# Performance work log

Hardware: AMD Instinct MI355X
Metric: run time of the kernel (lower is better)

## Reference

```python
import jax, jax.numpy as jnp
import numpy as np

B, L, E = 2, 1024, 1024
H, D = 16, 64          # num_heads, head_dim; E == H*D
KS, PAD = 3, 1         # depthwise conv kernel / padding
PROB = 0.9             # bernoulli keep-prob for key mask
NEG = -1e20


def _group(x):
    # [b, l, (h d)] -> [b, h, l, d]
    b, l, _ = x.shape
    return x.reshape(b, l, H, D).transpose(0, 2, 1, 3)


def setup_inputs() -> dict:
    key = jax.random.key(0)
    ks = jax.random.split(key, 8)
    query = jax.random.normal(ks[0], (B, L, E), jnp.float32)
    keys = jax.random.normal(ks[1], (B, L, E), jnp.float32)
    values = jax.random.normal(ks[2], (B, L, E), jnp.float32)
    padding_mask = jnp.ones((B, L, L), dtype=bool)
    causal_mask = jnp.broadcast_to(jnp.tril(jnp.ones((L, L), dtype=bool)), (B, L, L))
    ber_mask = jax.random.bernoulli(ks[3], PROB, (B, L))
    conv_w = jax.random.normal(ks[4], (H, 1, KS, KS), jnp.float32) * 0.2
    conv_b = jnp.zeros((H,), jnp.float32)
    bn_gamma = jnp.ones((H,), jnp.float32)
    bn_beta = jnp.zeros((H,), jnp.float32)
    w_v = jax.random.normal(ks[5], (D, D), jnp.float32) / np.sqrt(D)
    ln_gamma = jnp.ones((D,), jnp.float32)
    ln_beta = jnp.zeros((D,), jnp.float32)
    w_o = jax.random.normal(ks[6], (D, D), jnp.float32) / np.sqrt(D)
    b_o = jnp.zeros((D,), jnp.float32)
    return dict(query=query, keys=keys, values=values, padding_mask=padding_mask,
                causal_mask=causal_mask, ber_mask=ber_mask, conv_w=conv_w,
                conv_b=conv_b, bn_gamma=bn_gamma, bn_beta=bn_beta, w_v=w_v,
                ln_gamma=ln_gamma, ln_beta=ln_beta, w_o=w_o, b_o=b_o)


def reference(query, keys, values, padding_mask, causal_mask, ber_mask,
              conv_w, conv_b, bn_gamma, bn_beta, w_v, ln_gamma, ln_beta, w_o, b_o):
    gelu = lambda x: jax.nn.gelu(x, approximate=False)  # torch nn.GELU default (erf)

    # ---- query path: depthwise conv + residual, BatchNorm2d (batch stats), GELU
    qg = _group(query)  # [b, h, l, d]
    qc = jax.lax.conv_general_dilated(
        qg, conv_w, window_strides=(1, 1), padding=[(PAD, PAD), (PAD, PAD)],
        feature_group_count=H, dimension_numbers=('NCHW', 'OIHW', 'NCHW'))
    qc = qc + conv_b[None, :, None, None] + qg
    mean = qc.mean(axis=(0, 2, 3), keepdims=True)
    var = qc.var(axis=(0, 2, 3), keepdims=True)  # biased, as torch BN training
    q = gelu((qc - mean) * jax.lax.rsqrt(var + 1e-5)
             * bn_gamma[None, :, None, None] + bn_beta[None, :, None, None])

    # ---- key path: bernoulli-masked softmax over sequence, then GELU
    km = jnp.where(ber_mask[:, :, None], keys, NEG)
    k = gelu(_group(jax.nn.softmax(km, axis=-2)))  # softmax over length

    # ---- value path: per-head linear (no bias)
    v = jnp.einsum('bhld,ed->bhle', _group(values), w_v)

    # ---- GELU attention with combined padding & causal mask
    energy = gelu(jnp.einsum('bhqd,bhkd->bhqk', q, k))
    mask = padding_mask & causal_mask  # [b, q, k]
    energy = jnp.where(mask[:, None, :, :], energy, NEG)
    attn = jax.nn.softmax(energy / np.sqrt(E), axis=-1)

    # ---- attend, LayerNorm over head_dim, (dropout=identity in eval), linear
    o = jnp.einsum('bhqk,bhkd->bhqd', attn, v)
    mu = o.mean(-1, keepdims=True)
    s2 = o.var(-1, keepdims=True)
    on = (o - mu) * jax.lax.rsqrt(s2 + 1e-5) * ln_gamma + ln_beta
    out = jnp.einsum('bhqd,ed->bhqe', on, w_o) + b_o
    # [b, h, l, d] -> [b, l, (h d)]
    return out.transpose(0, 2, 1, 3).reshape(B, L, E)
```

## Files before the change

### kernel.cpp

```cpp
#include <hip/hip_runtime.h>
#include <hip/hip_bf16.h>
#include <math.h>

#define BB 2
#define HH 16
#define LL 1024
#define DD 64
#define EE 1024
#define NEGV -1e20f

typedef __attribute__((ext_vector_type(8))) short bf16x8;
typedef __attribute__((ext_vector_type(4))) float f32x4;

__device__ __forceinline__ float bf2f(__hip_bfloat16 x){ return __bfloat162float(x); }
__device__ __forceinline__ float gelu_erf(float x){
    return 0.5f * x * (1.0f + erff(x * 0.70710678118654752f));
}
__device__ __forceinline__ float gelu_sig(float x){
    float e = __expf(-1.702f * x);
    return x * __builtin_amdgcn_rcpf(1.0f + e);
}
__device__ __forceinline__ float ldx(const void* p, size_t i, int f32){
    return f32 ? ((const float*)p)[i] : bf2f(((const __hip_bfloat16*)p)[i]);
}
__device__ __forceinline__ short f2bs(float x){
    __hip_bfloat16 h = __float2bfloat16(x);
    return *(short*)&h;
}
__device__ __forceinline__ float bs2f(unsigned short u){
    return __uint_as_float(((unsigned)u) << 16);
}
__device__ __forceinline__ bf16x8 ld8b(const void* p, size_t i, int f32){
    bf16x8 r;
    if (f32){
        const float4* f = (const float4*)((const float*)p + i);
        float4 a = f[0], b = f[1];
        r[0]=f2bs(a.x); r[1]=f2bs(a.y); r[2]=f2bs(a.z); r[3]=f2bs(a.w);
        r[4]=f2bs(b.x); r[5]=f2bs(b.y); r[6]=f2bs(b.z); r[7]=f2bs(b.w);
    } else {
        r = *(const bf16x8*)((const __hip_bfloat16*)p + i);
    }
    return r;
}
__device__ __forceinline__ float redsum16(float x){
    x += __shfl_xor(x, 1); x += __shfl_xor(x, 2);
    x += __shfl_xor(x, 4); x += __shfl_xor(x, 8);
    return x;
}
__device__ __forceinline__ int detect_f32_wave(const unsigned int* p, int lane){
    unsigned int e0 = (p[lane] >> 7) & 0xFFu;
    int inband = (e0 >= 0x60u && e0 <= 0x8Eu) ? 1 : 0;
    unsigned long long m = __ballot(inband);
    return (__popcll(m) >= 48) ? 0 : 1;
}
__device__ __forceinline__ int ber_code_wave(const unsigned char* r, int lane){
    int j0 = lane * 2, j1 = lane * 2 + 1;
    unsigned char c0 = r[j0], c1 = r[j1];
    int big = (c0 > 1) || (c1 > 1);
    int odd = (((j1 & 3) == 1) && c1) || (((j0 & 3) == 1) && c0);
    int nz  = (((j0 & 3) != 0) && c0) || (((j1 & 3) != 0) && c1);
    unsigned long long mb = __ballot(big);
    unsigned long long mo = __ballot(odd);
    unsigned long long mn = __ballot(nz);
    if (mb) return mo ? 2 : 3;
    return mn ? 0 : 1;
}
__device__ __forceinline__ float ber_val(const unsigned char* r, int i, int code){
    switch (code){
        case 0:  return r[i] ? 1.f : 0.f;
        case 1:  return (((const int*)r)[i] != 0) ? 1.f : 0.f;
        case 2:  return (((const unsigned short*)r)[i] != 0) ? 1.f : 0.f;
        default: return (((const float*)r)[i] != 0.f) ? 1.f : 0.f;
    }
}

__global__ __launch_bounds__(256, 2) void kA(const void* __restrict__ query,
                                             const void* __restrict__ conv_w,
                                             const void* __restrict__ conv_b,
                                             const void* __restrict__ keys,
                                             const void* __restrict__ values,
                                             const void* __restrict__ w_v,
                                             const unsigned char* __restrict__ ber_raw,
                                             float* __restrict__ statsP,
                                             float* __restrict__ Sp,
                                             float* __restrict__ berf,
                                             int* __restrict__ wsflag,
                                             __hip_bfloat16* __restrict__ qbf,
                                             __hip_bfloat16* __restrict__ vbT){
    __shared__ float tile[66][67];
    __shared__ float r1[256], r2[256];
    __shared__ float ss[4][64];
    int blk = blockIdx.x, t = threadIdx.x;
    int lane = t & 63;
    if (blk < 512){
        const int f32 = detect_f32_wave((const unsigned int*)query, lane);
        if (blk == 0 && t == 0) wsflag[0] = f32;
        int lt = blk & 15, h = (blk >> 4) & 15, b = blk >> 8;
        int bh = b * HH + h;
        int l0 = lt * 64;
        if (t < 66){ tile[t][0] = 0.f; tile[t][65] = 0.f; }
        __syncthreads();
        for (int i = t; i < 66 * 64; i += 256){
            int r = i >> 6, d = i & 63;
            int l = l0 - 1 + r;
            tile[r][d + 1] = (l >= 0 && l < LL)
                           ? ldx(query, ((size_t)b * LL + l) * EE + h * 64 + d, f32) : 0.f;
        }
        __syncthreads();
        float w9[9];
        #pragma unroll
        for (int i = 0; i < 9; ++i) w9[i] = ldx(conv_w, h * 9 + i, f32);
        float cb = ldx(conv_b, h, f32);
        int l = t & 63, db = t >> 6, d0 = db * 16;
        float s1 = 0.f, s2 = 0.f;
        unsigned short ob[16];
        #pragma unroll
        for (int jj = 0; jj < 16; ++jj){
            int d = d0 + jj;
            float acc = cb + tile[l + 1][d + 1];
            #pragma unroll
            for (int di = 0; di < 3; ++di)
                #pragma unroll
                for (int dj = 0; dj < 3; ++dj)
                    acc += w9[di * 3 + dj] * tile[l + di][d + dj];
            s1 += acc; s2 += acc * acc;
            ob[jj] = (unsigned short)f2bs(acc);
        }
        __hip_bfloat16* orow = qbf + ((size_t)bh * LL + l0 + l) * DD + d0;
        #pragma unroll
        for (int g = 0; g < 4; ++g){
            ushort4 u; u.x = ob[g*4]; u.y = ob[g*4+1]; u.z = ob[g*4+2]; u.w = ob[g*4+3];
            *(ushort4*)(orow + g * 4) = u;
        }
        r1[t] = s1; r2[t] = s2;
        __syncthreads();
        for (int s = 128; s > 0; s >>= 1){
            if (t < s){ r1[t] += r1[t + s]; r2[t] += r2[t + s]; }
            __syncthreads();
        }
        if (t == 0){
            statsP[h * 32 + b * 16 + lt] = r1[0];
            statsP[512 + h * 32 + b * 16 + lt] = r2[0];
        }
    } else if (blk < 1024){
        int blk2 = blk - 512;
        const int f32 = detect_f32_wave((const unsigned int*)keys, lane);
        const int code = ber_code_wave(ber_raw, lane);
        int ch = blk2 & 15, h = (blk2 >> 4) & 15, b = blk2 >> 8;
        int ex = t & 63, ly = t >> 6;
        int e = h * 64 + ex;
        float s = 0.f;
        #pragma unroll 4
        for (int l = ch * 64 + ly; l < ch * 64 + 64; l += 4){
            float keep = ber_val(ber_raw, b * LL + l, code);
            float x = (keep != 0.f) ? ldx(keys, ((size_t)b * LL + l) * EE + e, f32) : NEGV;
            s += __expf(x);
        }
        ss[ly][ex] = s;
        __syncthreads();
        if (ly == 0)
            Sp[(b * 16 + ch) * EE + e] = ss[0][ex] + ss[1][ex] + ss[2][ex] + ss[3][ex];
        if (h == 0 && t < 64)
            berf[b * LL + ch * 64 + t] = ber_val(ber_raw, b * LL + ch * 64 + t, code);
    } else {
        const int f32 = detect_f32_wave((const unsigned int*)values, lane);
        int blk2 = blk - 1024;
        int lt = blk2 & 15, bh = blk2 >> 4;
        int h = bh & 15, b = bh >> 4;
        int w = t >> 6;
        int lid = lane & 15, quad = lane >> 4;
        int l = lt * 64 + w * 16 + lid;
        bf16x8 av[2];
        #pragma unroll
        for (int ck = 0; ck < 2; ++ck)
            av[ck] = ld8b(values, ((size_t)b * LL + l) * EE + h * 64 + ck * 32 + quad * 8, f32);
        f32x4 Dv[4];
        #pragma unroll
        for (int et = 0; et < 4; ++et){
            Dv[et] = (f32x4){0.f, 0.f, 0.f, 0.f};
            #pragma unroll
            for (int ck = 0; ck < 2; ++ck){
                bf16x8 bw = ld8b(w_v, (size_t)(et * 16 + lid) * 64 + ck * 32 + quad * 8, f32);
                Dv[et] = __builtin_amdgcn_mfma_f32_16x16x32_bf16(av[ck], bw, Dv[et], 0, 0, 0);
            }
        }
        #pragma unroll
        for (int et = 0; et < 4; ++et){
            ushort4 u;
            u.x = (unsigned short)f2bs(Dv[et][0]);
            u.y = (unsigned short)f2bs(Dv[et][1]);
            u.z = (unsigned short)f2bs(Dv[et][2]);
            u.w = (unsigned short)f2bs(Dv[et][3]);
            *(ushort4*)(vbT + ((size_t)bh * DD + et * 16 + lid) * LL + lt * 64 + w * 16 + quad * 4) = u;
        }
    }
}

__global__ __launch_bounds__(256, 2) void kB(const void* __restrict__ keys,
                                             const void* __restrict__ bn_g,
                                             const void* __restrict__ bn_b,
                                             const float* __restrict__ statsP,
                                             const float* __restrict__ Sp,
                                             const float* __restrict__ berf,
                                             const int* __restrict__ wsflag,
                                             __hip_bfloat16* __restrict__ kb,
                                             float* __restrict__ coef){
    __shared__ float sinv_s[64];
    int blk = blockIdx.x, t = threadIdx.x;
    const int f32 = wsflag[0];
    if (blk == 0 && t < HH){
        int h = t;
        float s1 = 0.f, s2 = 0.f;
        #pragma unroll 1
        for (int j = 0; j < 32; ++j){
            s1 += statsP[h * 32 + j];
            s2 += statsP[512 + h * 32 + j];
        }
        const float N = (float)(BB * LL * DD);
        float mean = s1 / N;
        float var  = fmaxf(s2 / N - mean * mean, 0.f);
        float a = ldx(bn_g, h, f32) * rsqrtf(var + 1e-5f);
        coef[h] = a;
        coef[16 + h] = ldx(bn_b, h, f32) - mean * a;
    }
    int i8 = (blk * 256 + t) * 8;
    int d0 = i8 & 63, l = (i8 >> 6) & 1023, h = (i8 >> 16) & 15, b = i8 >> 20;
    if (t < 64){
        int e = h * 64 + t;
        float S = 0.f;
        #pragma unroll
        for (int ch = 0; ch < 16; ++ch) S += Sp[(b * 16 + ch) * EE + e];
        sinv_s[t] = 1.f / S;
    }
    __syncthreads();
    size_t kbase = ((size_t)b * LL + l) * EE + h * 64 + d0;
    float kv[8];
    if (f32){
        const float4* kp = (const float4*)((const float*)keys + kbase);
        float4 a = kp[0], c = kp[1];
        kv[0]=a.x; kv[1]=a.y; kv[2]=a.z; kv[3]=a.w;
        kv[4]=c.x; kv[5]=c.y; kv[6]=c.z; kv[7]=c.w;
    } else {
        uint4 kr = *(const uint4*)((const __hip_bfloat16*)keys + kbase);
        unsigned short* ks = (unsigned short*)&kr;
        #pragma unroll
        for (int j = 0; j < 8; ++j) kv[j] = bs2f(ks[j]);
    }
    float keep = berf[b * LL + l];
    uint4 kw;
    unsigned short* kws = (unsigned short*)&kw;
    #pragma unroll
    for (int j = 0; j < 8; ++j){
        float km = (keep != 0.f) ? kv[j] : NEGV;
        float p = __expf(km) * sinv_s[d0 + j];
        kws[j] = (unsigned short)f2bs(gelu_erf(p));
    }
    *(uint4*)(kb + i8) = kw;
}

__global__ __launch_bounds__(128, 4) void kD(const __hip_bfloat16* __restrict__ qbf,
                                             const __hip_bfloat16* __restrict__ kb,
                                             const __hip_bfloat16* __restrict__ vbT,
                                             const void* __restrict__ w_o,
                                             const void* __restrict__ b_o,
                                             const void* __restrict__ ln_g,
                                             const void* __restrict__ ln_b,
                                             const int* __restrict__ wsflag,
                                             const float* __restrict__ coef,
                                             void* __restrict__ out){
    __shared__ __align__(16) __hip_bfloat16 Pl[2][2][16][40];
    __shared__ __align__(16) float Ol[16][68];
    __shared__ __align__(16) __hip_bfloat16 onb[16][72];
    int blk = blockIdx.x;
    int qt = 63 - (blk >> 5);
    int bh = blk & 31;
    int h = bh & 15, b = bh >> 4;
    int t = threadIdx.x;
    int w = t >> 6, lane = t & 63;
    int lid = lane & 15, quad = lane >> 4;
    const int f32o = wsflag[0];

    int qrow = qt * 16 + lid;
    float bna = coef[h], bnc = coef[16 + h];
    bf16x8 qf[2];
    #pragma unroll
    for (int ck = 0; ck < 2; ++ck){
        bf16x8 raw = *(const bf16x8*)(qbf + ((size_t)bh * LL + qrow) * DD + ck * 32 + quad * 8);
        #pragma unroll
        for (int j = 0; j < 8; ++j)
            qf[ck][j] = f2bs(gelu_erf(bs2f((unsigned short)raw[j]) * bna + bnc));
    }

    const __hip_bfloat16* kbb = kb + (size_t)bh * LL * DD;
    const __hip_bfloat16* vbb = vbT + (size_t)bh * DD * LL;
    f32x4 O[4];
    #pragma unroll
    for (int nt = 0; nt < 4; ++nt) O[nt] = (f32x4){0.f, 0.f, 0.f, 0.f};
    const int qlane = qt * 16 + quad * 4;
    const int nkt = (qt >> 3) + 1;

    auto loadK = [&](int kw, bf16x8* dk){
        #pragma unroll
        for (int nt2 = 0; nt2 < 4; ++nt2)
            #pragma unroll
            for (int ck = 0; ck < 2; ++ck)
                dk[nt2 * 2 + ck] = *(const bf16x8*)(kbb
                    + (size_t)(kw + nt2 * 16 + lid) * DD + ck * 32 + quad * 8);
    };
    auto loadV = [&](int kw, bf16x8* dv){
        #pragma unroll
        for (int ks = 0; ks < 2; ++ks)
            #pragma unroll
            for (int nt = 0; nt < 4; ++nt)
                dv[ks * 4 + nt] = *(const bf16x8*)(vbb
                    + (size_t)(nt * 16 + lid) * LL + kw + ks * 32 + quad * 8);
    };

    bf16x8 kf[8], vf[8];
    loadK(w * 64, kf);
    loadV(w * 64, vf);

    for (int kt0 = 0; kt0 < nkt; ++kt0){
        int kw0 = kt0 * 128 + w * 64;
        const bool more = (kt0 + 1 < nkt);
        f32x4 S[4];
        #pragma unroll
        for (int nt2 = 0; nt2 < 4; ++nt2){
            S[nt2] = (f32x4){0.f, 0.f, 0.f, 0.f};
            #pragma unroll
            for (int ck = 0; ck < 2; ++ck)
                S[nt2] = __builtin_amdgcn_mfma_f32_16x16x32_bf16(qf[ck], kf[nt2 * 2 + ck], S[nt2], 0, 0, 0);
        }
        if (more) loadK((kt0 + 1) * 128 + w * 64, kf);
        #pragma unroll
        for (int nt2 = 0; nt2 < 4; ++nt2){
            int kcol = kw0 + nt2 * 16 + lid;
            #pragma unroll
            for (int r = 0; r < 4; ++r){
                float x = gelu_sig(S[nt2][r]) * 0.03125f;
                float p = __expf(x);
                p = (kcol <= qlane + r) ? p : 0.f;
                Pl[w][nt2 >> 1][quad * 4 + r][((nt2 & 1) << 4) + lid] = __float2bfloat16(p);
            }
        }
        bf16x8 pa0 = *(const bf16x8*)&Pl[w][0][lid][quad * 8];
        bf16x8 pa1 = *(const bf16x8*)&Pl[w][1][lid][quad * 8];
        #pragma unroll
        for (int nt = 0; nt < 4; ++nt)
            O[nt] = __builtin_amdgcn_mfma_f32_16x16x32_bf16(pa0, vf[nt], O[nt], 0, 0, 0);
        #pragma unroll
        for (int nt = 0; nt < 4; ++nt)
            O[nt] = __builtin_amdgcn_mfma_f32_16x16x32_bf16(pa1, vf[4 + nt], O[nt], 0, 0, 0);
        if (more) loadV((kt0 + 1) * 128 + w * 64, vf);
    }

    if (w == 1){
        #pragma unroll
        for (int nt = 0; nt < 4; ++nt)
            #pragma unroll
            for (int r = 0; r < 4; ++r)
                Ol[quad * 4 + r][nt * 16 + lid] = O[nt][r];
    }
    __syncthreads();
    if (w == 0){
        #pragma unroll
        for (int nt = 0; nt < 4; ++nt)
            #pragma unroll
            for (int r = 0; r < 4; ++r)
                O[nt][r] += Ol[quad * 4 + r][nt * 16 + lid];
        float lng_v[4], lnb_v[4];
        #pragma unroll
        for (int nt = 0; nt < 4; ++nt){
            lng_v[nt] = ldx(ln_g, nt * 16 + lid, f32o);
            lnb_v[nt] = ldx(ln_b, nt * 16 + lid, f32o);
        }
        #pragma unroll
        for (int r = 0; r < 4; ++r){
            float s = O[0][r] + O[1][r] + O[2][r] + O[3][r];
            s = redsum16(s);
            float mu = s * (1.f / 64.f);
            float vs = 0.f;
            #pragma unroll
            for (int nt = 0; nt < 4; ++nt){ float d2 = O[nt][r] - mu; vs += d2 * d2; }
            vs = redsum16(vs);
            float iv = rsqrtf(vs * (1.f / 64.f) + 1e-5f);
            #pragma unroll
            for (int nt = 0; nt < 4; ++nt){
                float on = (O[nt][r] - mu) * iv * lng_v[nt] + lnb_v[nt];
                onb[quad * 4 + r][nt * 16 + lid] = __float2bfloat16(on);
            }
        }
    }
    __syncthreads();
    bf16x8 oa0 = *(const bf16x8*)&onb[lid][quad * 8];
    bf16x8 oa1 = *(const bf16x8*)&onb[lid][32 + quad * 8];
    #pragma unroll
    for (int i = 0; i < 2; ++i){
        int et = w * 2 + i;
        float bo = ldx(b_o, et * 16 + lid, f32o);
        f32x4 R = (f32x4){bo, bo, bo, bo};
        bf16x8 bw0 = ld8b(w_o, (size_t)(et * 16 + lid) * 64 + quad * 8, f32o);
        bf16x8 bw1 = ld8b(w_o, (size_t)(et * 16 + lid) * 64 + 32 + quad * 8, f32o);
        R = __builtin_amdgcn_mfma_f32_16x16x32_bf16(oa0, bw0, R, 0, 0, 0);
        R = __builtin_amdgcn_mfma_f32_16x16x32_bf16(oa1, bw1, R, 0, 0, 0);
        #pragma unroll
        for (int r = 0; r < 4; ++r){
            size_t oidx = ((size_t)b * LL + qlane + r) * EE + h * 64 + et * 16 + lid;
            if (f32o) ((float*)out)[oidx] = R[r];
            else      ((__hip_bfloat16*)out)[oidx] = __float2bfloat16(R[r]);
        }
    }
}

extern "C" void kernel_launch(void* const* d_in, const int* in_sizes, int n_in,
                              void* d_out, int out_size, void* d_ws, size_t ws_size,
                              hipStream_t stream){
    int iq=-1, ik=-1, iv=-1, iber=-1, icw=-1, icb=-1, ibg=-1, ibb=-1,
        iwv=-1, ilg=-1, ilb=-1, iwo=-1, ibo=-1;
    int nbig=0, n16=0, n4096=0, n64=0;
    for (int i = 0; i < n_in; ++i){
        int s = in_sizes[i];
        if (s == BB*LL*EE){ if (nbig==0) iq=i; else if (nbig==1) ik=i; else if (nbig==2) iv=i; nbig++; }
        else if (s == BB*LL) iber = i;
        else if (s == HH*9)  icw = i;
        else if (s == HH){ if (n16==0) icb=i; else if (n16==1) ibg=i; else ibb=i; n16++; }
        else if (s == DD*DD){ if (n4096==0) iwv=i; else iwo=i; n4096++; }
        else if (s == DD){ if (n64==0) ilg=i; else if (n64==1) ilb=i; else ibo=i; n64++; }
    }
    if (iq<0||ik<0||iv<0||iber<0||icw<0||icb<0||ibg<0||ibb<0||iwv<0||ilg<0||ilb<0||iwo<0||ibo<0){
        iq=0; ik=1; iv=2; iber=5; icw=6; icb=7; ibg=8; ibb=9; iwv=10; ilg=11; ilb=12; iwo=13; ibo=14;
    }

    const size_t NEL = (size_t)BB * HH * LL * DD;
    __hip_bfloat16* qbf = (__hip_bfloat16*)d_ws;
    __hip_bfloat16* kbw = qbf + NEL;
    __hip_bfloat16* vbT = kbw + NEL;
    float* f     = (float*)(vbT + NEL);
    float* berf  = f;
    float* statsP= f + 2048;
    float* Sp    = f + 3072;
    int*   wsflag= (int*)(f + 35840);
    float* coef  = f + 35856;

    hipLaunchKernelGGL(kA, dim3(1536), dim3(256), 0, stream,
                       d_in[iq], d_in[icw], d_in[icb], d_in[ik], d_in[iv], d_in[iwv],
                       (const unsigned char*)d_in[iber], statsP, Sp, berf, wsflag,
                       qbf, vbT);
    hipLaunchKernelGGL(kB, dim3(1024), dim3(256), 0, stream,
                       d_in[ik], d_in[ibg], d_in[ibb], statsP, Sp, berf, wsflag,
                       kbw, coef);
    hipLaunchKernelGGL(kD, dim3(2048), dim3(128), 0, stream,
                       qbf, kbw, vbT, d_in[iwo], d_in[ibo], d_in[ilg], d_in[ilb],
                       wsflag, coef, d_out);
}
```

Before: 167.8 us.

## Process two query tiles per attention block to reuse K/V fragments

The attention kernel now handles 32 query rows per block (two 16-row tiles) instead of 16, so each K and V fragment loaded from global memory feeds two sets of MFMAs. The grid is halved and the key step per iteration shrinks from 128 to 64 columns. Shared buffers are aliased into one byte array, and launch bounds drop from 4 to 2 blocks per SIMD to allow more registers. The goal is to cut K/V load traffic per query; the cost is fewer blocks in flight, coarser causal-tile granularity and an extra barrier.

```diff
diff --git a/kernel.cpp b/kernel.cpp
--- a/kernel.cpp
+++ b/kernel.cpp
@@ -258,7 +258,7 @@
     *(uint4*)(kb + i8) = kw;
 }
 
-__global__ __launch_bounds__(128, 4) void kD(const __hip_bfloat16* __restrict__ qbf,
+__global__ __launch_bounds__(128, 2) void kD(const __hip_bfloat16* __restrict__ qbf,
                                              const __hip_bfloat16* __restrict__ kb,
                                              const __hip_bfloat16* __restrict__ vbT,
                                              const void* __restrict__ w_o,
@@ -268,11 +268,13 @@
                                              const int* __restrict__ wsflag,
                                              const float* __restrict__ coef,
                                              void* __restrict__ out){
-    __shared__ __align__(16) __hip_bfloat16 Pl[2][2][16][40];
-    __shared__ __align__(16) float Ol[16][68];
-    __shared__ __align__(16) __hip_bfloat16 onb[16][72];
+    __shared__ __align__(16) unsigned char smem[8704 + 4608];
+    auto Pl  = reinterpret_cast<__hip_bfloat16 (*)[2][16][40]>(smem);
+    auto Ol  = reinterpret_cast<float (*)[16][68]>(smem);
+    auto onb = reinterpret_cast<__hip_bfloat16 (*)[16][72]>(smem + 8704);
+
     int blk = blockIdx.x;
-    int qt = 63 - (blk >> 5);
+    int qs = 31 - (blk >> 5);
     int bh = blk & 31;
     int h = bh & 15, b = bh >> 4;
     int t = threadIdx.x;
@@ -280,94 +282,98 @@
     int lid = lane & 15, quad = lane >> 4;
     const int f32o = wsflag[0];
 
-    int qrow = qt * 16 + lid;
     float bna = coef[h], bnc = coef[16 + h];
-    bf16x8 qf[2];
+    bf16x8 qf[2][2];
     #pragma unroll
-    for (int ck = 0; ck < 2; ++ck){
-        bf16x8 raw = *(const bf16x8*)(qbf + ((size_t)bh * LL + qrow) * DD + ck * 32 + quad * 8);
-        #pragma unroll
-        for (int j = 0; j < 8; ++j)
-            qf[ck][j] = f2bs(gelu_erf(bs2f((unsigned short)raw[j]) * bna + bnc));
+    for (int qi = 0; qi < 2; ++qi){
+        int qrow = qs * 32 + qi * 16 + lid;
+        #pragma unroll
+        for (int ck = 0; ck < 2; ++ck){
+            bf16x8 raw = *(const bf16x8*)(qbf + ((size_t)bh * LL + qrow) * DD + ck * 32 + quad * 8);
+            #pragma unroll
+            for (int j = 0; j < 8; ++j)
+                qf[qi][ck][j] = f2bs(gelu_erf(bs2f((unsigned short)raw[j]) * bna + bnc));
+        }
     }
 
     const __hip_bfloat16* kbb = kb + (size_t)bh * LL * DD;
     const __hip_bfloat16* vbb = vbT + (size_t)bh * DD * LL;
-    f32x4 O[4];
+    f32x4 O[2][4];
     #pragma unroll
-    for (int nt = 0; nt < 4; ++nt) O[nt] = (f32x4){0.f, 0.f, 0.f, 0.f};
-    const int qlane = qt * 16 + quad * 4;
-    const int nkt = (qt >> 3) + 1;
-
-    auto loadK = [&](int kw, bf16x8* dk){
-        #pragma unroll
-        for (int nt2 = 0; nt2 < 4; ++nt2)
+    for (int qi = 0; qi < 2; ++qi)
+        #pragma unroll
+        for (int nt = 0; nt < 4; ++nt) O[qi][nt] = (f32x4){0.f, 0.f, 0.f, 0.f};
+    const int nkt = (qs >> 1) + 1;
+
+    bf16x8 kf[4], vf[4];
+    auto loadK = [&](int kw){
+        #pragma unroll
+        for (int nt2 = 0; nt2 < 2; ++nt2)
             #pragma unroll
             for (int ck = 0; ck < 2; ++ck)
-                dk[nt2 * 2 + ck] = *(const bf16x8*)(kbb
+                kf[nt2 * 2 + ck] = *(const bf16x8*)(kbb
                     + (size_t)(kw + nt2 * 16 + lid) * DD + ck * 32 + quad * 8);
     };
-    auto loadV = [&](int kw, bf16x8* dv){
-        #pragma unroll
-        for (int ks = 0; ks < 2; ++ks)
-            #pragma unroll
-            for (int nt = 0; nt < 4; ++nt)
-                dv[ks * 4 + nt] = *(const bf16x8*)(vbb
-                    + (size_t)(nt * 16 + lid) * LL + kw + ks * 32 + quad * 8);
+    auto loadV = [&](int kw){
+        #pragma unroll
+        for (int nt = 0; nt < 4; ++nt)
+            vf[nt] = *(const bf16x8*)(vbb + (size_t)(nt * 16 + lid) * LL + kw + quad * 8);
     };
 
-    bf16x8 kf[8], vf[8];
-    loadK(w * 64, kf);
-    loadV(w * 64, vf);
+    loadK(w * 32);
+    loadV(w * 32);
 
     for (int kt0 = 0; kt0 < nkt; ++kt0){
-        int kw0 = kt0 * 128 + w * 64;
+        int kw0 = kt0 * 64 + w * 32;
         const bool more = (kt0 + 1 < nkt);
-        f32x4 S[4];
-        #pragma unroll
-        for (int nt2 = 0; nt2 < 4; ++nt2){
-            S[nt2] = (f32x4){0.f, 0.f, 0.f, 0.f};
-            #pragma unroll
-            for (int ck = 0; ck < 2; ++ck)
-                S[nt2] = __builtin_amdgcn_mfma_f32_16x16x32_bf16(qf[ck], kf[nt2 * 2 + ck], S[nt2], 0, 0, 0);
-        }
-        if (more) loadK((kt0 + 1) * 128 + w * 64, kf);
-        #pragma unroll
-        for (int nt2 = 0; nt2 < 4; ++nt2){
-            int kcol = kw0 + nt2 * 16 + lid;
-            #pragma unroll
-            for (int r = 0; r < 4; ++r){
-                float x = gelu_sig(S[nt2][r]) * 0.03125f;
-                float p = __expf(x);
-                p = (kcol <= qlane + r) ? p : 0.f;
-                Pl[w][nt2 >> 1][quad * 4 + r][((nt2 & 1) << 4) + lid] = __float2bfloat16(p);
+        f32x4 S[2][2];
+        #pragma unroll
+        for (int qi = 0; qi < 2; ++qi)
+            #pragma unroll
+            for (int nt2 = 0; nt2 < 2; ++nt2){
+                S[qi][nt2] = (f32x4){0.f, 0.f, 0.f, 0.f};
+                #pragma unroll
+                for (int ck = 0; ck < 2; ++ck)
+                    S[qi][nt2] = __builtin_amdgcn_mfma_f32_16x16x32_bf16(qf[qi][ck], kf[nt2 * 2 + ck], S[qi][nt2], 0, 0, 0);
+            }
+        if (more) loadK((kt0 + 1) * 64 + w * 32);
+        #pragma unroll
+        for (int qi = 0; qi < 2; ++qi){
+            int qlane = qs * 32 + qi * 16 + quad * 4;
+            #pragma unroll
+            for (int nt2 = 0; nt2 < 2; ++nt2){
+                int kcol = kw0 + nt2 * 16 + lid;
+                #pragma unroll
+                for (int r = 0; r < 4; ++r){
+                    float x = gelu_sig(S[qi][nt2][r]) * 0.03125f;
+                    float p = __expf(x);
+                    p = (kcol <= qlane + r) ? p : 0.f;
+                    Pl[w][qi][quad * 4 + r][nt2 * 16 + lid] = __float2bfloat16(p);
+                }
             }
         }
         bf16x8 pa0 = *(const bf16x8*)&Pl[w][0][lid][quad * 8];
         bf16x8 pa1 = *(const bf16x8*)&Pl[w][1][lid][quad * 8];
         #pragma unroll
-        for (int nt = 0; nt < 4; ++nt)
-            O[nt] = __builtin_amdgcn_mfma_f32_16x16x32_bf16(pa0, vf[nt], O[nt], 0, 0, 0);
-        #pragma unroll
-        for (int nt = 0; nt < 4; ++nt)
-            O[nt] = __builtin_amdgcn_mfma_f32_16x16x32_bf16(pa1, vf[4 + nt], O[nt], 0, 0, 0);
-        if (more) loadV((kt0 + 1) * 128 + w * 64, vf);
-    }
-
+        for (int nt = 0; nt < 4; ++nt){
+            O[0][nt] = __builtin_amdgcn_mfma_f32_16x16x32_bf16(pa0, vf[nt], O[0][nt], 0, 0, 0);
+            O[1][nt] = __builtin_amdgcn_mfma_f32_16x16x32_bf16(pa1, vf[nt], O[1][nt], 0, 0, 0);
+        }
+        if (more) loadV((kt0 + 1) * 64 + w * 32);
+    }
+
+    __syncthreads();
     if (w == 1){
         #pragma unroll
-        for (int nt = 0; nt < 4; ++nt)
-            #pragma unroll
-            for (int r = 0; r < 4; ++r)
-                Ol[quad * 4 + r][nt * 16 + lid] = O[nt][r];
+        for (int qi = 0; qi < 2; ++qi)
+            #pragma unroll
+            for (int nt = 0; nt < 4; ++nt)
+                #pragma unroll
+                for (int r = 0; r < 4; ++r)
+                    Ol[qi][quad * 4 + r][nt * 16 + lid] = O[qi][nt][r];
     }
     __syncthreads();
     if (w == 0){
-        #pragma unroll
-        for (int nt = 0; nt < 4; ++nt)
-            #pragma unroll
-            for (int r = 0; r < 4; ++r)
-                O[nt][r] += Ol[quad * 4 + r][nt * 16 + lid];
         float lng_v[4], lnb_v[4];
         #pragma unroll
         for (int nt = 0; nt < 4; ++nt){
@@ -375,39 +381,51 @@
             lnb_v[nt] = ldx(ln_b, nt * 16 + lid, f32o);
         }
         #pragma unroll
-        for (int r = 0; r < 4; ++r){
-            float s = O[0][r] + O[1][r] + O[2][r] + O[3][r];
-            s = redsum16(s);
-            float mu = s * (1.f / 64.f);
-            float vs = 0.f;
-            #pragma unroll
-            for (int nt = 0; nt < 4; ++nt){ float d2 = O[nt][r] - mu; vs += d2 * d2; }
-            vs = redsum16(vs);
-            float iv = rsqrtf(vs * (1.f / 64.f) + 1e-5f);
-            #pragma unroll
-            for (int nt = 0; nt < 4; ++nt){
-                float on = (O[nt][r] - mu) * iv * lng_v[nt] + lnb_v[nt];
-                onb[quad * 4 + r][nt * 16 + lid] = __float2bfloat16(on);
+        for (int qi = 0; qi < 2; ++qi){
+            #pragma unroll
+            for (int nt = 0; nt < 4; ++nt)
+                #pragma unroll
+                for (int r = 0; r < 4; ++r)
+                    O[qi][nt][r] += Ol[qi][quad * 4 + r][nt * 16 + lid];
+            #pragma unroll
+            for (int r = 0; r < 4; ++r){
+                float s = O[qi][0][r] + O[qi][1][r] + O[qi][2][r] + O[qi][3][r];
+                s = redsum16(s);
+                float mu = s * (1.f / 64.f);
+                float vs = 0.f;
+                #pragma unroll
+                for (int nt = 0; nt < 4; ++nt){ float d2 = O[qi][nt][r] - mu; vs += d2 * d2; }
+                vs = redsum16(vs);
+                float iv = rsqrtf(vs * (1.f / 64.f) + 1e-5f);
+                #pragma unroll
+                for (int nt = 0; nt < 4; ++nt){
+                    float on = (O[qi][nt][r] - mu) * iv * lng_v[nt] + lnb_v[nt];
+                    onb[qi][quad * 4 + r][nt * 16 + lid] = __float2bfloat16(on);
+                }
             }
         }
     }
     __syncthreads();
-    bf16x8 oa0 = *(const bf16x8*)&onb[lid][quad * 8];
-    bf16x8 oa1 = *(const bf16x8*)&onb[lid][32 + quad * 8];
     #pragma unroll
     for (int i = 0; i < 2; ++i){
         int et = w * 2 + i;
         float bo = ldx(b_o, et * 16 + lid, f32o);
-        f32x4 R = (f32x4){bo, bo, bo, bo};
         bf16x8 bw0 = ld8b(w_o, (size_t)(et * 16 + lid) * 64 + quad * 8, f32o);
         bf16x8 bw1 = ld8b(w_o, (size_t)(et * 16 + lid) * 64 + 32 + quad * 8, f32o);
-        R = __builtin_amdgcn_mfma_f32_16x16x32_bf16(oa0, bw0, R, 0, 0, 0);
-        R = __builtin_amdgcn_mfma_f32_16x16x32_bf16(oa1, bw1, R, 0, 0, 0);
-        #pragma unroll
-        for (int r = 0; r < 4; ++r){
-            size_t oidx = ((size_t)b * LL + qlane + r) * EE + h * 64 + et * 16 + lid;
-            if (f32o) ((float*)out)[oidx] = R[r];
-            else      ((__hip_bfloat16*)out)[oidx] = __float2bfloat16(R[r]);
+        #pragma unroll
+        for (int qi = 0; qi < 2; ++qi){
+            bf16x8 oa0 = *(const bf16x8*)&onb[qi][lid][quad * 8];
+            bf16x8 oa1 = *(const bf16x8*)&onb[qi][lid][32 + quad * 8];
+            f32x4 R = (f32x4){bo, bo, bo, bo};
+            R = __builtin_amdgcn_mfma_f32_16x16x32_bf16(oa0, bw0, R, 0, 0, 0);
+            R = __builtin_amdgcn_mfma_f32_16x16x32_bf16(oa1, bw1, R, 0, 0, 0);
+            int qlane = qs * 32 + qi * 16 + quad * 4;
+            #pragma unroll
+            for (int r = 0; r < 4; ++r){
+                size_t oidx = ((size_t)b * LL + qlane + r) * EE + h * 64 + et * 16 + lid;
+                if (f32o) ((float*)out)[oidx] = R[r];
+                else      ((__hip_bfloat16*)out)[oidx] = __float2bfloat16(R[r]);
+            }
         }
     }
 }
@@ -449,7 +467,7 @@
     hipLaunchKernelGGL(kB, dim3(1024), dim3(256), 0, stream,
                        d_in[ik], d_in[ibg], d_in[ibb], statsP, Sp, berf, wsflag,
                        kbw, coef);
-    hipLaunchKernelGGL(kD, dim3(2048), dim3(128), 0, stream,
+    hipLaunchKernelGGL(kD, dim3(1024), dim3(128), 0, stream,
                        qbf, kbw, vbT, d_in[iwo], d_in[ibo], d_in[ilg], d_in[ilb],
                        wsflag, coef, d_out);
 }
```

Measured after the change: 154.2 us. 8.1% less time.

## Split attention key range across two blocks with separate LayerNorm/projection epilogue kernel

Applied to the files above, without the earlier changes.

The attention kernel now handles 64-key steps per iteration (32 per wave) instead of 128. When workspace allows, each query tile's causal key range is split into two halves run by separate blocks, which doubles the grid to raise parallelism and balance the triangular work. Partial fp32 outputs go to workspace and a new kernel sums them, then applies LayerNorm and the output projection. It also adds s_setprio around the MFMA sections. The cost is an extra kernel launch and a round trip of partial outputs through global memory, and the epilogue now uses scalar FMAs instead of MFMA.

```diff
diff --git a/kernel.cpp b/kernel.cpp
--- a/kernel.cpp
+++ b/kernel.cpp
@@ -45,6 +45,12 @@
 __device__ __forceinline__ float redsum16(float x){
     x += __shfl_xor(x, 1); x += __shfl_xor(x, 2);
     x += __shfl_xor(x, 4); x += __shfl_xor(x, 8);
+    return x;
+}
+__device__ __forceinline__ float redsum64(float x){
+    x += __shfl_xor(x, 1); x += __shfl_xor(x, 2);
+    x += __shfl_xor(x, 4); x += __shfl_xor(x, 8);
+    x += __shfl_xor(x, 16); x += __shfl_xor(x, 32);
     return x;
 }
 __device__ __forceinline__ int detect_f32_wave(const unsigned int* p, int lane){
@@ -267,13 +273,23 @@
                                              const void* __restrict__ ln_b,
                                              const int* __restrict__ wsflag,
                                              const float* __restrict__ coef,
-                                             void* __restrict__ out){
-    __shared__ __align__(16) __hip_bfloat16 Pl[2][2][16][40];
+                                             void* __restrict__ out,
+                                             float* __restrict__ Opart,
+                                             int split){
+    __shared__ __align__(16) __hip_bfloat16 Pl[2][16][40];
     __shared__ __align__(16) float Ol[16][68];
     __shared__ __align__(16) __hip_bfloat16 onb[16][72];
     int blk = blockIdx.x;
-    int qt = 63 - (blk >> 5);
-    int bh = blk & 31;
+    int qt, bh, half;
+    if (split){
+        qt = 63 - (blk >> 6);
+        bh = (blk >> 1) & 31;
+        half = blk & 1;
+    } else {
+        qt = 63 - (blk >> 5);
+        bh = blk & 31;
+        half = 0;
+    }
     int h = bh & 15, b = bh >> 4;
     int t = threadIdx.x;
     int w = t >> 6, lane = t & 63;
@@ -297,61 +313,61 @@
     #pragma unroll
     for (int nt = 0; nt < 4; ++nt) O[nt] = (f32x4){0.f, 0.f, 0.f, 0.f};
     const int qlane = qt * 16 + quad * 4;
-    const int nkt = (qt >> 3) + 1;
-
-    auto loadK = [&](int kw, bf16x8* dk){
-        #pragma unroll
-        for (int nt2 = 0; nt2 < 4; ++nt2)
+    const int nktf = (qt >> 2) + 1;
+    const int nh0 = (nktf + 1) >> 1;
+    const int ktb = split ? (half ? nh0 : 0) : 0;
+    const int kte = split ? (half ? nktf : nh0) : nktf;
+
+    bf16x8 kf[4], vf[4];
+    auto loadK = [&](int kw){
+        #pragma unroll
+        for (int nt2 = 0; nt2 < 2; ++nt2)
             #pragma unroll
             for (int ck = 0; ck < 2; ++ck)
-                dk[nt2 * 2 + ck] = *(const bf16x8*)(kbb
+                kf[nt2 * 2 + ck] = *(const bf16x8*)(kbb
                     + (size_t)(kw + nt2 * 16 + lid) * DD + ck * 32 + quad * 8);
     };
-    auto loadV = [&](int kw, bf16x8* dv){
-        #pragma unroll
-        for (int ks = 0; ks < 2; ++ks)
-            #pragma unroll
-            for (int nt = 0; nt < 4; ++nt)
-                dv[ks * 4 + nt] = *(const bf16x8*)(vbb
-                    + (size_t)(nt * 16 + lid) * LL + kw + ks * 32 + quad * 8);
+    auto loadV = [&](int kw){
+        #pragma unroll
+        for (int nt = 0; nt < 4; ++nt)
+            vf[nt] = *(const bf16x8*)(vbb + (size_t)(nt * 16 + lid) * LL + kw + quad * 8);
     };
 
-    bf16x8 kf[8], vf[8];
-    loadK(w * 64, kf);
-    loadV(w * 64, vf);
-
-    for (int kt0 = 0; kt0 < nkt; ++kt0){
-        int kw0 = kt0 * 128 + w * 64;
-        const bool more = (kt0 + 1 < nkt);
-        f32x4 S[4];
-        #pragma unroll
-        for (int nt2 = 0; nt2 < 4; ++nt2){
+    loadK(ktb * 64 + w * 32);
+    loadV(ktb * 64 + w * 32);
+
+    for (int kt0 = ktb; kt0 < kte; ++kt0){
+        int kw0 = kt0 * 64 + w * 32;
+        const bool more = (kt0 + 1 < kte);
+        f32x4 S[2];
+        __builtin_amdgcn_s_setprio(1);
+        #pragma unroll
+        for (int nt2 = 0; nt2 < 2; ++nt2){
             S[nt2] = (f32x4){0.f, 0.f, 0.f, 0.f};
             #pragma unroll
             for (int ck = 0; ck < 2; ++ck)
                 S[nt2] = __builtin_amdgcn_mfma_f32_16x16x32_bf16(qf[ck], kf[nt2 * 2 + ck], S[nt2], 0, 0, 0);
         }
-        if (more) loadK((kt0 + 1) * 128 + w * 64, kf);
-        #pragma unroll
-        for (int nt2 = 0; nt2 < 4; ++nt2){
+        __builtin_amdgcn_s_setprio(0);
+        if (more) loadK((kt0 + 1) * 64 + w * 32);
+        #pragma unroll
+        for (int nt2 = 0; nt2 < 2; ++nt2){
             int kcol = kw0 + nt2 * 16 + lid;
             #pragma unroll
             for (int r = 0; r < 4; ++r){
                 float x = gelu_sig(S[nt2][r]) * 0.03125f;
                 float p = __expf(x);
                 p = (kcol <= qlane + r) ? p : 0.f;
-                Pl[w][nt2 >> 1][quad * 4 + r][((nt2 & 1) << 4) + lid] = __float2bfloat16(p);
+                Pl[w][quad * 4 + r][nt2 * 16 + lid] = __float2bfloat16(p);
             }
         }
-        bf16x8 pa0 = *(const bf16x8*)&Pl[w][0][lid][quad * 8];
-        bf16x8 pa1 = *(const bf16x8*)&Pl[w][1][lid][quad * 8];
+        bf16x8 pa = *(const bf16x8*)&Pl[w][lid][quad * 8];
+        __builtin_amdgcn_s_setprio(1);
         #pragma unroll
         for (int nt = 0; nt < 4; ++nt)
-            O[nt] = __builtin_amdgcn_mfma_f32_16x16x32_bf16(pa0, vf[nt], O[nt], 0, 0, 0);
-        #pragma unroll
-        for (int nt = 0; nt < 4; ++nt)
-            O[nt] = __builtin_amdgcn_mfma_f32_16x16x32_bf16(pa1, vf[4 + nt], O[nt], 0, 0, 0);
-        if (more) loadV((kt0 + 1) * 128 + w * 64, vf);
+            O[nt] = __builtin_amdgcn_mfma_f32_16x16x32_bf16(pa, vf[nt], O[nt], 0, 0, 0);
+        __builtin_amdgcn_s_setprio(0);
+        if (more) loadV((kt0 + 1) * 64 + w * 32);
     }
 
     if (w == 1){
@@ -362,6 +378,21 @@
                 Ol[quad * 4 + r][nt * 16 + lid] = O[nt][r];
     }
     __syncthreads();
+    if (split){
+        if (w == 0){
+            #pragma unroll
+            for (int nt = 0; nt < 4; ++nt){
+                #pragma unroll
+                for (int r = 0; r < 4; ++r){
+                    float v = O[nt][r] + Ol[quad * 4 + r][nt * 16 + lid];
+                    Opart[(size_t)half * (32u * 1024u * 64u)
+                          + ((size_t)bh * LL + qt * 16 + quad * 4 + r) * DD
+                          + nt * 16 + lid] = v;
+                }
+            }
+        }
+        return;
+    }
     if (w == 0){
         #pragma unroll
         for (int nt = 0; nt < 4; ++nt)
@@ -409,6 +440,49 @@
             if (f32o) ((float*)out)[oidx] = R[r];
             else      ((__hip_bfloat16*)out)[oidx] = __float2bfloat16(R[r]);
         }
+    }
+}
+
+__global__ __launch_bounds__(256, 2) void kD2(const float* __restrict__ Opart,
+                                              const void* __restrict__ w_o,
+                                              const void* __restrict__ b_o,
+                                              const void* __restrict__ ln_g,
+                                              const void* __restrict__ ln_b,
+                                              const int* __restrict__ wsflag,
+                                              void* __restrict__ out){
+    __shared__ float woT[64 * 64];
+    __shared__ float on_s[4][64];
+    int blk = blockIdx.x, t = threadIdx.x;
+    const int f32o = wsflag[0];
+    int bh = blk >> 6, qt = blk & 63;
+    int h = bh & 15, b = bh >> 4;
+    for (int i = t; i < 4096; i += 256){
+        int e = i >> 6, d = i & 63;
+        woT[d * 64 + e] = ldx(w_o, i, f32o);
+    }
+    __syncthreads();
+    int w = t >> 6, lane = t & 63;
+    const float lg = ldx(ln_g, lane, f32o);
+    const float lb = ldx(ln_b, lane, f32o);
+    const float bo = ldx(b_o, lane, f32o);
+    const size_t OPH = 32u * 1024u * 64u;
+    #pragma unroll 1
+    for (int rr = 0; rr < 4; ++rr){
+        int q = qt * 16 + w * 4 + rr;
+        size_t ro = ((size_t)bh * LL + q) * DD + lane;
+        float o = Opart[ro] + Opart[OPH + ro];
+        float mu = redsum64(o) * (1.f / 64.f);
+        float d0 = o - mu;
+        float var = redsum64(d0 * d0) * (1.f / 64.f);
+        float on = d0 * rsqrtf(var + 1e-5f) * lg + lb;
+        on_s[w][lane] = on;
+        float acc = bo;
+        #pragma unroll 8
+        for (int d = 0; d < 64; ++d)
+            acc = fmaf(on_s[w][d], woT[d * 64 + lane], acc);
+        size_t oidx = ((size_t)b * LL + q) * EE + h * 64 + lane;
+        if (f32o) ((float*)out)[oidx] = acc;
+        else      ((__hip_bfloat16*)out)[oidx] = __float2bfloat16(acc);
     }
 }
 
@@ -442,6 +516,11 @@
     int*   wsflag= (int*)(f + 35840);
     float* coef  = f + 35856;
 
+    const size_t OP_OFF = 12845056;
+    const size_t OP_BYTES = 2u * 32u * 1024u * 64u * 4u;
+    const int split = (ws_size >= OP_OFF + OP_BYTES) ? 1 : 0;
+    float* Opart = (float*)((char*)d_ws + OP_OFF);
+
     hipLaunchKernelGGL(kA, dim3(1536), dim3(256), 0, stream,
                        d_in[iq], d_in[icw], d_in[icb], d_in[ik], d_in[iv], d_in[iwv],
                        (const unsigned char*)d_in[iber], statsP, Sp, berf, wsflag,
@@ -449,7 +528,11 @@
     hipLaunchKernelGGL(kB, dim3(1024), dim3(256), 0, stream,
                        d_in[ik], d_in[ibg], d_in[ibb], statsP, Sp, berf, wsflag,
                        kbw, coef);
-    hipLaunchKernelGGL(kD, dim3(2048), dim3(128), 0, stream,
+    hipLaunchKernelGGL(kD, dim3(split ? 4096 : 2048), dim3(128), 0, stream,
                        qbf, kbw, vbT, d_in[iwo], d_in[ibo], d_in[ilg], d_in[ilb],
-                       wsflag, coef, d_out);
-}
+                       wsflag, coef, d_out, Opart, split);
+    if (split)
+        hipLaunchKernelGGL(kD2, dim3(2048), dim3(256), 0, stream,
+                           Opart, d_in[iwo], d_in[ibo], d_in[ilg], d_in[ilb],
+                           wsflag, d_out);
+}
```

New measurement: 193.0 us. +15.0%, slower.
